# Performance work log

Hardware: AMD Instinct MI355X
Metric: run time of the kernel (lower is better)

Reference implementation:

```python
import jax, jax.numpy as jnp
import numpy as np
import math

EPS = 1e-5

def _ln(x, g, b):
    m = jnp.mean(x, axis=-1, keepdims=True)
    v = jnp.var(x, axis=-1, keepdims=True)
    return (x - m) * jax.lax.rsqrt(v + EPS) * g + b

def _rn_layer(x, W, g, b, A, Bb, Rw):
    # x: (B,S,in) -> (B,S,out). W: (out,in), A: (out,basis), Bb: (basis,out)
    S = x.shape[1]
    basis_dim = Bb.shape[0]
    n = _ln(x @ W.T, g, b)                      # (B,S,out)
    j = jnp.arange(S) % basis_dim               # (S,)
    Bv = Bb[j]                                  # (S,out)
    scal = jnp.einsum('bsd,sd->bs', n, Bv)      # (B,S)
    Av = A[:, j].T                              # (S,out)
    nf = scal[..., None] * Av                   # (B,S,out)
    res = x if Rw is None else x @ Rw.T
    return nf + res

def _ts_layer(x, M, g, b, P, Rw):
    # x: (B,S,in) -> (B,S,out). M: (out,in), P: (out,out,G)
    S = x.shape[1]
    D, _, G = P.shape
    t = _ln(x @ M.T, g, b)                      # (B,S,out)
    k = jnp.arange(S, dtype=jnp.float32)
    periods = (jnp.arange(D, dtype=jnp.float32)[:, None, None] * (D * G)
               + jnp.arange(D, dtype=jnp.float32)[None, :, None] * G
               + jnp.arange(G, dtype=jnp.float32)[None, None, :] + 2.0)  # (D,D,G)
    phi = jnp.cos(2.0 * math.pi * k[:, None, None, None] / periods)       # (S,D,D,G)
    # Nk[b,s,i] = sum_{j,g} P[i,j,g] * t[b,s,j] * phi[s,i,j,g]
    Wp = jnp.einsum('ijg,sijg->sij', P, phi)    # (S,D,D)
    Nk = jnp.einsum('sij,bsj->bsi', Wp, t)      # (B,S,D)
    return Nk + x @ Rw.T

def setup_inputs() -> dict:
    key = jax.random.key(0)
    ks = jax.random.split(key, 16)
    B, S = 2, 2048
    d0, d1, d2 = 512, 64, 512        # input_dim, ts out, final out
    bas1, G, bas3 = 64, 8, 64
    u = lambda k, sh, a: jax.random.uniform(k, sh, jnp.float32, -a, a)
    inp = {
        'x':  jax.random.normal(ks[0], (B, S, d0), jnp.float32),
        # Layer 1: RN 512->512 (in==out -> no residual proj)
        'W1': u(ks[1], (d0, d0), 0.1),
        'g1': jnp.ones((d0,), jnp.float32),
        'b1': jnp.zeros((d0,), jnp.float32),
        'A1': u(ks[2], (d0, bas1), 0.1),
        'B1': u(ks[3], (bas1, d0), 0.1),
        # Layer 2: TS 512->64
        'M2': u(ks[4], (d1, d0), 0.5),
        'g2': jnp.ones((d1,), jnp.float32),
        'b2': jnp.zeros((d1,), jnp.float32),
        'P2': u(ks[5], (d1, d1, G), 0.1),
        'R2': u(ks[6], (d1, d0), 0.1),
        # Layer 3: RN 64->512
        'W3': u(ks[7], (d2, d1), 0.1),
        'g3': jnp.ones((d2,), jnp.float32),
        'b3': jnp.zeros((d2,), jnp.float32),
        'A3': u(ks[8], (d2, bas3), 0.1),
        'B3': u(ks[9], (bas3, d2), 0.1),
        'R3': u(ks[10], (d2, d1), 0.1),
    }
    return inp

def reference(x, W1, g1, b1, A1, B1, M2, g2, b2, P2, R2, W3, g3, b3, A3, B3, R3):
    h = _rn_layer(x, W1, g1, b1, A1, B1, None)   # (B,S,512), identity residual
    h = _ts_layer(h, M2, g2, b2, P2, R2)         # (B,S,64)
    h = _rn_layer(h, W3, g3, b3, A3, B3, R3)     # (B,S,512)
    return h
```

## Files before the change

### kernel.cpp

```cpp
#include <hip/hip_runtime.h>
#include <math.h>

#define SEQ  2048
#define ROWS 4096
#define D0   512
#define D1   64

typedef short bf8 __attribute__((ext_vector_type(8)));
typedef float f4  __attribute__((ext_vector_type(4)));

__device__ __forceinline__ unsigned short f2bf(float f) {
    unsigned u = __float_as_uint(f);
    return (unsigned short)((u + 0x7fffu + ((u >> 16) & 1u)) >> 16);
}
__device__ __forceinline__ float bf2f(unsigned short u) {
    return __uint_as_float((unsigned)u << 16);
}
__device__ __forceinline__ void hilo(float f, unsigned short& h, unsigned short& l) {
    h = f2bf(f);
    float fh = bf2f(h);
    l = f2bf(f - fh);
}
__device__ __forceinline__ void cv4h(unsigned short* dh, int idx, float4 v) {
    ushort4 hv;
    hv.x = f2bf(v.x); hv.y = f2bf(v.y); hv.z = f2bf(v.z); hv.w = f2bf(v.w);
    *(ushort4*)(dh + idx) = hv;
}

__device__ __forceinline__ void async16(const void* g, void* l) {
    __builtin_amdgcn_global_load_lds(
        (const __attribute__((address_space(1))) unsigned int*)g,
        (__attribute__((address_space(3))) unsigned int*)l, 16, 0, 0);
}

__global__ __launch_bounds__(256) void convk(
        const float* __restrict__ x,  const float* __restrict__ W1,
        const float* __restrict__ M2, const float* __restrict__ R2,
        const float* __restrict__ W3, const float* __restrict__ R3,
        const float* __restrict__ A1, const float* __restrict__ A3,
        unsigned short* __restrict__ xh,
        unsigned short* __restrict__ W1h,
        unsigned short* __restrict__ C2h,
        unsigned short* __restrict__ C3h,
        float* __restrict__ A1T, float* __restrict__ A3T) {
    int c = blockIdx.x, tid = threadIdx.x;
    if (c < 1216) {
        const float* src; unsigned short* dh; int off;
        if      (c < 1024) { src = x;  dh = xh;          off = c; }
        else if (c < 1152) { src = W1; dh = W1h;         off = c - 1024; }
        else if (c < 1168) { src = M2; dh = C2h;         off = c - 1152; }
        else if (c < 1184) { src = R2; dh = C2h + 32768; off = c - 1168; }
        else if (c < 1200) { src = W3; dh = C3h;         off = c - 1184; }
        else               { src = R3; dh = C3h + 32768; off = c - 1200; }
        int base = off * 2048 + tid * 4;
        cv4h(dh, base,        *(const float4*)(src + base));
        cv4h(dh, base + 1024, *(const float4*)(src + base + 1024));
    } else {
        int gid = (c - 1216) * 256 + tid;
        int i = gid >> 6, j = gid & 63;
        A1T[j * 512 + i] = A1[gid];
        A3T[j * 512 + i] = A3[gid];
    }
}

template<bool ALO, int OM>
__global__ __launch_bounds__(256, 4) void gemm128t(
        const unsigned short* __restrict__ Ah, const unsigned short* __restrict__ Al,
        const unsigned short* __restrict__ Wh,
        float* __restrict__ Cf, unsigned short* __restrict__ Cb,
        int M, int N, int K, int Ks) {
    __shared__ __align__(16) unsigned short aH[8192];
    __shared__ __align__(16) unsigned short aL[ALO ? 8192 : 16];
    __shared__ __align__(16) unsigned short wH[4096];
    const int tid = threadIdx.x;
    const int wv  = tid >> 6;
    const int ln  = tid & 63;
    const int lm  = ln & 15;
    const int lq  = ln >> 4;
    const int bm  = blockIdx.y * 128;
    const int bn  = blockIdx.x * 64;
    const int k0  = blockIdx.z * Ks;

    f4 acc[2][4] = {};

    for (int kt = 0; kt < Ks; kt += 64) {
        const int kg = k0 + kt;
        __syncthreads();
#pragma unroll
        for (int i = 0; i < 4; ++i) {
            int slot = i * 256 + wv * 64 + ln;
            int row  = slot >> 3;
            int ch   = (slot & 7) ^ (row & 7);
            size_t go = (size_t)(bm + row) * K + kg + ch * 8;
            async16(Ah + go, aH + slot * 8);
            if constexpr (ALO) async16(Al + go, aL + slot * 8);
        }
#pragma unroll
        for (int i = 0; i < 2; ++i) {
            int slot = i * 256 + wv * 64 + ln;
            int row  = slot >> 3;
            int ch   = (slot & 7) ^ (row & 7);
            size_t go = (size_t)(bn + row) * K + kg + ch * 8;
            async16(Wh + go, wH + slot * 8);
        }
        __syncthreads();

#pragma unroll
        for (int kk = 0; kk < 2; ++kk) {
            const int ck = kk * 4 + lq;
            bf8 a_h[2], a_l[2], b_h[4];
#pragma unroll
            for (int t = 0; t < 2; ++t) {
                int r = wv * 32 + t * 16 + lm;
                a_h[t] = *(const bf8*)(aH + r * 64 + ((ck ^ (r & 7)) * 8));
                if constexpr (ALO)
                    a_l[t] = *(const bf8*)(aL + r * 64 + ((ck ^ (r & 7)) * 8));
            }
#pragma unroll
            for (int u = 0; u < 4; ++u) {
                int rb = u * 16 + lm;
                b_h[u] = *(const bf8*)(wH + rb * 64 + ((ck ^ (rb & 7)) * 8));
            }
#pragma unroll
            for (int t = 0; t < 2; ++t)
#pragma unroll
                for (int u = 0; u < 4; ++u) {
                    acc[t][u] = __builtin_amdgcn_mfma_f32_16x16x32_bf16(a_h[t], b_h[u], acc[t][u], 0, 0, 0);
                    if constexpr (ALO)
                        acc[t][u] = __builtin_amdgcn_mfma_f32_16x16x32_bf16(a_l[t], b_h[u], acc[t][u], 0, 0, 0);
                }
        }
    }

#pragma unroll
    for (int t = 0; t < 2; ++t)
#pragma unroll
        for (int u = 0; u < 4; ++u) {
            int row = bm + wv * 32 + t * 16 + lq * 4;
            int col = bn + u * 16 + lm;
#pragma unroll
            for (int r = 0; r < 4; ++r) {
                float v = acc[t][u][r];
                if constexpr (OM == 0) {
                    Cf[(size_t)blockIdx.z * M * N + (size_t)(row + r) * N + col] = v;
                } else if constexpr (OM == 1) {
                    Cb[(size_t)blockIdx.z * M * N + (size_t)(row + r) * N + col] = f2bf(v);
                } else {
                    if (col < 512) Cb[(size_t)(row + r) * 512 + col] = f2bf(v);
                    else           Cf[(size_t)(row + r) * 512 + col - 512] = v;
                }
            }
        }
}

__global__ __launch_bounds__(256) void lnrn(
        const unsigned short* __restrict__ Yb0,
        const unsigned short* __restrict__ Yb1,
        const float* __restrict__ RES,
        const float* __restrict__ g, const float* __restrict__ be,
        const float* __restrict__ Bb, const float* __restrict__ AaT,
        float* __restrict__ outf,
        unsigned short* __restrict__ outh, unsigned short* __restrict__ outl) {
    const int row = blockIdx.x * 4 + (threadIdx.x >> 6);
    const int l = threadIdx.x & 63;
    const int c = l * 8;
    ushort4 ua = *(const ushort4*)(Yb0 + (size_t)row * D0 + c);
    ushort4 ub = *(const ushort4*)(Yb0 + (size_t)row * D0 + c + 4);
    float4 y0, y1;
    y0.x = bf2f(ua.x); y0.y = bf2f(ua.y); y0.z = bf2f(ua.z); y0.w = bf2f(ua.w);
    y1.x = bf2f(ub.x); y1.y = bf2f(ub.y); y1.z = bf2f(ub.z); y1.w = bf2f(ub.w);
    if (Yb1) {
        ushort4 va = *(const ushort4*)(Yb1 + (size_t)row * D0 + c);
        ushort4 vb = *(const ushort4*)(Yb1 + (size_t)row * D0 + c + 4);
        y0.x += bf2f(va.x); y0.y += bf2f(va.y); y0.z += bf2f(va.z); y0.w += bf2f(va.w);
        y1.x += bf2f(vb.x); y1.y += bf2f(vb.y); y1.z += bf2f(vb.z); y1.w += bf2f(vb.w);
    }
    float sum = y0.x + y0.y + y0.z + y0.w + y1.x + y1.y + y1.z + y1.w;
    float ssq = y0.x*y0.x + y0.y*y0.y + y0.z*y0.z + y0.w*y0.w
              + y1.x*y1.x + y1.y*y1.y + y1.z*y1.z + y1.w*y1.w;
#pragma unroll
    for (int m = 1; m < 64; m <<= 1) {
        sum += __shfl_xor(sum, m, 64);
        ssq += __shfl_xor(ssq, m, 64);
    }
    float mean = sum * (1.0f / 512.0f);
    float var  = ssq * (1.0f / 512.0f) - mean * mean;
    float rstd = rsqrtf(var + 1e-5f);
    float4 g0 = *(const float4*)(g + c),  g1v = *(const float4*)(g + c + 4);
    float4 e0 = *(const float4*)(be + c), e1  = *(const float4*)(be + c + 4);
    float4 n0, n1;
    n0.x = (y0.x - mean) * rstd * g0.x  + e0.x;
    n0.y = (y0.y - mean) * rstd * g0.y  + e0.y;
    n0.z = (y0.z - mean) * rstd * g0.z  + e0.z;
    n0.w = (y0.w - mean) * rstd * g0.w  + e0.w;
    n1.x = (y1.x - mean) * rstd * g1v.x + e1.x;
    n1.y = (y1.y - mean) * rstd * g1v.y + e1.y;
    n1.z = (y1.z - mean) * rstd * g1v.z + e1.z;
    n1.w = (y1.w - mean) * rstd * g1v.w + e1.w;
    const int jm = row & 63;
    const float* bb = Bb + jm * D0 + c;
    float4 b0 = *(const float4*)bb, b1v = *(const float4*)(bb + 4);
    float p = n0.x*b0.x + n0.y*b0.y + n0.z*b0.z + n0.w*b0.w
            + n1.x*b1v.x + n1.y*b1v.y + n1.z*b1v.z + n1.w*b1v.w;
#pragma unroll
    for (int m = 1; m < 64; m <<= 1) p += __shfl_xor(p, m, 64);
    const float* av = AaT + jm * D0 + c;
    float4 a0 = *(const float4*)av, a1 = *(const float4*)(av + 4);
    const float* rs = RES + (size_t)row * D0 + c;
    float4 r0 = *(const float4*)rs, r1 = *(const float4*)(rs + 4);
    float4 v0, v1;
    v0.x = p*a0.x + r0.x; v0.y = p*a0.y + r0.y; v0.z = p*a0.z + r0.z; v0.w = p*a0.w + r0.w;
    v1.x = p*a1.x + r1.x; v1.y = p*a1.y + r1.y; v1.z = p*a1.z + r1.z; v1.w = p*a1.w + r1.w;
    if (outf) {
        *(float4*)(outf + (size_t)row * D0 + c)     = v0;
        *(float4*)(outf + (size_t)row * D0 + c + 4) = v1;
    } else {
        ushort4 h0, l0, h1, l1;
        hilo(v0.x, h0.x, l0.x); hilo(v0.y, h0.y, l0.y);
        hilo(v0.z, h0.z, l0.z); hilo(v0.w, h0.w, l0.w);
        hilo(v1.x, h1.x, l1.x); hilo(v1.y, h1.y, l1.y);
        hilo(v1.z, h1.z, l1.z); hilo(v1.w, h1.w, l1.w);
        *(ushort4*)(outh + (size_t)row * D0 + c)     = h0;
        *(ushort4*)(outl + (size_t)row * D0 + c)     = l0;
        *(ushort4*)(outh + (size_t)row * D0 + c + 4) = h1;
        *(ushort4*)(outl + (size_t)row * D0 + c + 4) = l1;
    }
}

#define C2S 524288
__global__ __launch_bounds__(256) void lnt(
        const float* __restrict__ C2, const float* __restrict__ g2,
        const float* __restrict__ b2,
        float* __restrict__ t, float* __restrict__ rsum) {
    const int r = blockIdx.x * 4 + (threadIdx.x >> 6);
    const int j = threadIdx.x & 63;
    size_t base = (size_t)r * 128 + j;
    float v = 0.f, rv = 0.f;
#pragma unroll
    for (int z = 0; z < 4; ++z) {
        v  += C2[(size_t)z * C2S + base];
        rv += C2[(size_t)z * C2S + base + 64];
    }
    float sum = v, ssq = v * v;
#pragma unroll
    for (int m = 1; m < 64; m <<= 1) {
        sum += __shfl_xor(sum, m, 64);
        ssq += __shfl_xor(ssq, m, 64);
    }
    float mean = sum * (1.0f / 64.0f);
    float var  = ssq * (1.0f / 64.0f) - mean * mean;
    float rstd = rsqrtf(var + 1e-5f);
    t[r * 64 + j]    = (v - mean) * rstd * g2[j] + b2[j];
    rsum[r * 64 + j] = rv;
}

__global__ __launch_bounds__(256) void tsk2(
        const float* __restrict__ t, const float* __restrict__ rsum,
        const float* __restrict__ P,
        unsigned short* __restrict__ Hh, unsigned short* __restrict__ Hl) {
    const int bid = blockIdx.x;
    const int i   = bid >> 3;
    const int sg  = bid & 7;
    const int w   = threadIdx.x >> 6;
    const int ln  = threadIdx.x & 63;
    const int s0  = sg * 256 + w * 64;
    const int idx = i * 64 + ln;
    const float* pp = P + idx * 8;
    const float sf0 = (float)s0;

    float k2c[8], ca[8], cb[8];
#pragma unroll
    for (int g = 0; g < 8; ++g) {
        float pf   = (float)(idx * 8 + g + 2);
        float invp = __builtin_amdgcn_rcpf(pf);
        k2c[g] = 2.0f * __builtin_amdgcn_cosf(invp);
        float q0 = floorf(sf0 * invp);
        float r0 = fmaf(-q0, pf, sf0);
        float f0 = r0 * invp; f0 -= floorf(f0);
        float c0 = __builtin_amdgcn_cosf(f0);
        float sf1 = sf0 + 1.0f;
        float q1 = floorf(sf1 * invp);
        float r1 = fmaf(-q1, pf, sf1);
        float f1 = r1 * invp; f1 -= floorf(f1);
        float c1 = __builtin_amdgcn_cosf(f1);
        float Pv = pp[g];
        ca[g] = Pv * c0;
        cb[g] = Pv * c1;
    }

    const int tb = s0 * 64 + ln;
    float t0c = t[tb], t1c = t[131072 + tb];
    float res0 = 0.f, res1 = 0.f;

    for (int st = 0; st < 64; st += 2) {
        float t0n  = t[tb + (st + 1) * 64];
        float t1n  = t[131072 + tb + (st + 1) * 64];
        float ws = ((ca[0] + ca[1]) + (ca[2] + ca[3]))
                 + ((ca[4] + ca[5]) + (ca[6] + ca[7]));
#pragma unroll
        for (int g = 0; g < 8; ++g) ca[g] = fmaf(k2c[g], cb[g], -ca[g]);
        float v0 = ws * t0c, v1 = ws * t1c;
#pragma unroll
        for (int m = 1; m < 64; m <<= 1) {
            v0 += __shfl_xor(v0, m, 64);
            v1 += __shfl_xor(v1, m, 64);
        }
        res0 = (ln == st) ? v0 : res0;
        res1 = (ln == st) ? v1 : res1;
        float t0n2 = t[tb + (st + 2) * 64];
        float t1n2 = t[131072 + tb + (st + 2) * 64];
        float ws2 = ((cb[0] + cb[1]) + (cb[2] + cb[3]))
                  + ((cb[4] + cb[5]) + (cb[6] + cb[7]));
#pragma unroll
        for (int g = 0; g < 8; ++g) cb[g] = fmaf(k2c[g], ca[g], -cb[g]);
        float v0b = ws2 * t0n, v1b = ws2 * t1n;
#pragma unroll
        for (int m = 1; m < 64; m <<= 1) {
            v0b += __shfl_xor(v0b, m, 64);
            v1b += __shfl_xor(v1b, m, 64);
        }
        res0 = (ln == st + 1) ? v0b : res0;
        res1 = (ln == st + 1) ? v1b : res1;
        t0c = t0n2; t1c = t1n2;
    }

    const int s = s0 + ln;
    {
        float v = res0 + rsum[(size_t)s * 64 + i];
        unsigned short h, l; hilo(v, h, l);
        Hh[(size_t)s * 64 + i] = h; Hl[(size_t)s * 64 + i] = l;
        float v1e = res1 + rsum[(size_t)(SEQ + s) * 64 + i];
        hilo(v1e, h, l);
        Hh[(size_t)(SEQ + s) * 64 + i] = h; Hl[(size_t)(SEQ + s) * 64 + i] = l;
    }
}

extern "C" void kernel_launch(void* const* d_in, const int* in_sizes, int n_in,
                              void* d_out, int out_size, void* d_ws, size_t ws_size,
                              hipStream_t stream) {
    const float* x  = (const float*)d_in[0];
    const float* W1 = (const float*)d_in[1];
    const float* g1 = (const float*)d_in[2];
    const float* b1 = (const float*)d_in[3];
    const float* A1 = (const float*)d_in[4];
    const float* B1 = (const float*)d_in[5];
    const float* M2 = (const float*)d_in[6];
    const float* g2 = (const float*)d_in[7];
    const float* b2 = (const float*)d_in[8];
    const float* P2 = (const float*)d_in[9];
    const float* R2 = (const float*)d_in[10];
    const float* W3 = (const float*)d_in[11];
    const float* g3 = (const float*)d_in[12];
    const float* b3 = (const float*)d_in[13];
    const float* A3 = (const float*)d_in[14];
    const float* B3 = (const float*)d_in[15];
    const float* R3 = (const float*)d_in[16];

    float* ws = (float*)d_ws;
    float* C2   = ws;
    float* C3r  = ws + 2097152;
    float* t    = ws + 4194304;
    float* rsum = ws + 4456448;
    float* A1T  = ws + 4718592;
    float* A3T  = ws + 4751360;
    unsigned short* us = (unsigned short*)(ws + 4784128);
    unsigned short* xh   = us;
    unsigned short* h1h  = us + 2097152;
    unsigned short* h1l  = us + 4194304;
    unsigned short* W1h  = us + 6291456;
    unsigned short* Wc2h = us + 6553600;
    unsigned short* Wc3h = us + 6619136;
    unsigned short* h2h  = us + 6684672;
    unsigned short* h2l  = us + 6946816;
    unsigned short* C1b  = us + 7208960;
    unsigned short* C3n  = us + 11403264;

    dim3 blk(256);

    convk<<<1344, blk, 0, stream>>>(x, W1, M2, R2, W3, R3, A1, A3,
                                    xh, W1h, Wc2h, Wc3h, A1T, A3T);

    gemm128t<false, 1><<<dim3(8, 32, 2), blk, 0, stream>>>(
        xh, xh, W1h, nullptr, C1b, ROWS, 512, 512, 256);
    lnrn<<<1024, blk, 0, stream>>>(C1b, C1b + (size_t)ROWS * 512, x,
                                   g1, b1, B1, A1T, nullptr, h1h, h1l);

    gemm128t<true, 0><<<dim3(2, 32, 4), blk, 0, stream>>>(
        h1h, h1l, Wc2h, C2, nullptr, ROWS, 128, 512, 128);
    lnt<<<1024, blk, 0, stream>>>(C2, g2, b2, t, rsum);
    tsk2<<<512, blk, 0, stream>>>(t, rsum, P2, h2h, h2l);

    gemm128t<true, 2><<<dim3(16, 32, 1), blk, 0, stream>>>(
        h2h, h2l, Wc3h, C3r, C3n, ROWS, 1024, 64, 64);
    lnrn<<<1024, blk, 0, stream>>>(C3n, nullptr, C3r, g3, b3, B3, A3T,
                                   (float*)d_out, nullptr, nullptr);
}
```

Before: 152.1 us.

## Fold layer-1 output algebraically into layer-2 GEMM via precomputed A1·M2 products

Layer 1's output h1 = x + scal·A1[:,j] is linear in x, so its product with the layer-2 weights M2/R2 becomes x·M2ᵀ plus scal times a precomputed 64x64 table G = A1ᵀ·M2 (built inside the conversion kernel). One GEMM now computes both x·W1ᵀ and x·[M2;R2]ᵀ together, and a new fused kernel does LN1, the scalar projection, and LN2. This removes the h1 hi/lo materialization, a separate GEMM launch and the lnt kernel. In exchange, x is split into hi/lo bf16, with the lo pass applied only to the M2/R2 column blocks. A runtime branch replaces the compile-time low-part switch in the GEMM.

```diff
diff --git a/kernel.cpp b/kernel.cpp
--- a/kernel.cpp
+++ b/kernel.cpp
@@ -5,6 +5,7 @@
 #define ROWS 4096
 #define D0   512
 #define D1   64
+#define C2S  524288
 
 typedef short bf8 __attribute__((ext_vector_type(8)));
 typedef float f4  __attribute__((ext_vector_type(4)));
@@ -38,16 +39,28 @@
         const float* __restrict__ M2, const float* __restrict__ R2,
         const float* __restrict__ W3, const float* __restrict__ R3,
         const float* __restrict__ A1, const float* __restrict__ A3,
-        unsigned short* __restrict__ xh,
+        unsigned short* __restrict__ xh, unsigned short* __restrict__ xl,
         unsigned short* __restrict__ W1h,
         unsigned short* __restrict__ C2h,
         unsigned short* __restrict__ C3h,
-        float* __restrict__ A1T, float* __restrict__ A3T) {
+        float* __restrict__ A3T,
+        float* __restrict__ G2y, float* __restrict__ G2r) {
+    __shared__ float sh[4][64];
     int c = blockIdx.x, tid = threadIdx.x;
-    if (c < 1216) {
+    if (c < 1024) {
+        int base = c * 2048 + tid * 4;
+        float4 v0 = *(const float4*)(x + base);
+        float4 v1 = *(const float4*)(x + base + 1024);
+        ushort4 h, l;
+        hilo(v0.x, h.x, l.x); hilo(v0.y, h.y, l.y);
+        hilo(v0.z, h.z, l.z); hilo(v0.w, h.w, l.w);
+        *(ushort4*)(xh + base) = h; *(ushort4*)(xl + base) = l;
+        hilo(v1.x, h.x, l.x); hilo(v1.y, h.y, l.y);
+        hilo(v1.z, h.z, l.z); hilo(v1.w, h.w, l.w);
+        *(ushort4*)(xh + base + 1024) = h; *(ushort4*)(xl + base + 1024) = l;
+    } else if (c < 1216) {
         const float* src; unsigned short* dh; int off;
-        if      (c < 1024) { src = x;  dh = xh;          off = c; }
-        else if (c < 1152) { src = W1; dh = W1h;         off = c - 1024; }
+        if      (c < 1152) { src = W1; dh = W1h;         off = c - 1024; }
         else if (c < 1168) { src = M2; dh = C2h;         off = c - 1152; }
         else if (c < 1184) { src = R2; dh = C2h + 32768; off = c - 1168; }
         else if (c < 1200) { src = W3; dh = C3h;         off = c - 1184; }
@@ -55,23 +68,36 @@
         int base = off * 2048 + tid * 4;
         cv4h(dh, base,        *(const float4*)(src + base));
         cv4h(dh, base + 1024, *(const float4*)(src + base + 1024));
-    } else {
+    } else if (c < 1344) {
         int gid = (c - 1216) * 256 + tid;
         int i = gid >> 6, j = gid & 63;
-        A1T[j * 512 + i] = A1[gid];
         A3T[j * 512 + i] = A3[gid];
-    }
-}
-
-template<bool ALO, int OM>
+    } else {
+        int jrow = (c - 1344) & 63;
+        const float* wv = (c < 1408) ? (M2 + jrow * 512) : (R2 + jrow * 512);
+        float* G = (c < 1408) ? G2y : G2r;
+        int jm = tid & 63, q = tid >> 6;
+        const float* ap = A1 + (q * 128) * 64 + jm;
+        const float* wp = wv + q * 128;
+        float acc = 0.f;
+        for (int cc = 0; cc < 128; ++cc)
+            acc = fmaf(ap[cc * 64], wp[cc], acc);
+        sh[q][jm] = acc;
+        __syncthreads();
+        if (tid < 64)
+            G[tid * 64 + jrow] = (sh[0][tid] + sh[1][tid]) + (sh[2][tid] + sh[3][tid]);
+    }
+}
+
+template<int AMODE, int OM>
 __global__ __launch_bounds__(256, 4) void gemm128t(
         const unsigned short* __restrict__ Ah, const unsigned short* __restrict__ Al,
         const unsigned short* __restrict__ Wh,
         float* __restrict__ Cf, unsigned short* __restrict__ Cb,
-        int M, int N, int K, int Ks) {
+        int N, int K, int Ks) {
     __shared__ __align__(16) unsigned short aH[8192];
-    __shared__ __align__(16) unsigned short aL[ALO ? 8192 : 16];
-    __shared__ __align__(16) unsigned short wH[4096];
+    __shared__ __align__(16) unsigned short aL[AMODE ? 8192 : 16];
+    __shared__ __align__(16) unsigned short wHs[4096];
     const int tid = threadIdx.x;
     const int wv  = tid >> 6;
     const int ln  = tid & 63;
@@ -80,6 +106,7 @@
     const int bm  = blockIdx.y * 128;
     const int bn  = blockIdx.x * 64;
     const int k0  = blockIdx.z * Ks;
+    const bool alo = (AMODE == 1) || (AMODE == 2 && bn >= 512);
 
     f4 acc[2][4] = {};
 
@@ -93,7 +120,7 @@
             int ch   = (slot & 7) ^ (row & 7);
             size_t go = (size_t)(bm + row) * K + kg + ch * 8;
             async16(Ah + go, aH + slot * 8);
-            if constexpr (ALO) async16(Al + go, aL + slot * 8);
+            if (alo) async16(Al + go, aL + slot * 8);
         }
 #pragma unroll
         for (int i = 0; i < 2; ++i) {
@@ -101,7 +128,7 @@
             int row  = slot >> 3;
             int ch   = (slot & 7) ^ (row & 7);
             size_t go = (size_t)(bn + row) * K + kg + ch * 8;
-            async16(Wh + go, wH + slot * 8);
+            async16(Wh + go, wHs + slot * 8);
         }
         __syncthreads();
 
@@ -113,20 +140,20 @@
             for (int t = 0; t < 2; ++t) {
                 int r = wv * 32 + t * 16 + lm;
                 a_h[t] = *(const bf8*)(aH + r * 64 + ((ck ^ (r & 7)) * 8));
-                if constexpr (ALO)
+                if (alo)
                     a_l[t] = *(const bf8*)(aL + r * 64 + ((ck ^ (r & 7)) * 8));
             }
 #pragma unroll
             for (int u = 0; u < 4; ++u) {
                 int rb = u * 16 + lm;
-                b_h[u] = *(const bf8*)(wH + rb * 64 + ((ck ^ (rb & 7)) * 8));
+                b_h[u] = *(const bf8*)(wHs + rb * 64 + ((ck ^ (rb & 7)) * 8));
             }
 #pragma unroll
             for (int t = 0; t < 2; ++t)
 #pragma unroll
                 for (int u = 0; u < 4; ++u) {
                     acc[t][u] = __builtin_amdgcn_mfma_f32_16x16x32_bf16(a_h[t], b_h[u], acc[t][u], 0, 0, 0);
-                    if constexpr (ALO)
+                    if (alo)
                         acc[t][u] = __builtin_amdgcn_mfma_f32_16x16x32_bf16(a_l[t], b_h[u], acc[t][u], 0, 0, 0);
                 }
         }
@@ -141,26 +168,95 @@
 #pragma unroll
             for (int r = 0; r < 4; ++r) {
                 float v = acc[t][u][r];
-                if constexpr (OM == 0) {
-                    Cf[(size_t)blockIdx.z * M * N + (size_t)(row + r) * N + col] = v;
-                } else if constexpr (OM == 1) {
-                    Cb[(size_t)blockIdx.z * M * N + (size_t)(row + r) * N + col] = f2bf(v);
-                } else {
+                if constexpr (OM == 2) {
                     if (col < 512) Cb[(size_t)(row + r) * 512 + col] = f2bf(v);
                     else           Cf[(size_t)(row + r) * 512 + col - 512] = v;
+                } else {
+                    if (col < 512)
+                        Cb[(size_t)blockIdx.z * ROWS * 512 + (size_t)(row + r) * 512 + col] = f2bf(v);
+                    else
+                        Cf[(size_t)blockIdx.z * ROWS * 128 + (size_t)(row + r) * 128 + (col - 512)] = v;
                 }
             }
         }
 }
 
+__global__ __launch_bounds__(256) void ptk(
+        const unsigned short* __restrict__ C1b,
+        const float* __restrict__ C2,
+        const float* __restrict__ B1,
+        const float* __restrict__ g1, const float* __restrict__ b1,
+        const float* __restrict__ g2, const float* __restrict__ b2,
+        const float* __restrict__ G2y, const float* __restrict__ G2r,
+        float* __restrict__ t, float* __restrict__ rsum) {
+    const int row = blockIdx.x * 4 + (threadIdx.x >> 6);
+    const int l = threadIdx.x & 63;
+    const int c = l * 8;
+    const int jm = row & 63;
+    const size_t rb0 = (size_t)row * 512 + c;
+    ushort4 ua = *(const ushort4*)(C1b + rb0);
+    ushort4 ub = *(const ushort4*)(C1b + rb0 + 4);
+    ushort4 va = *(const ushort4*)(C1b + (size_t)ROWS * 512 + rb0);
+    ushort4 vb = *(const ushort4*)(C1b + (size_t)ROWS * 512 + rb0 + 4);
+    float y[8];
+    y[0] = bf2f(ua.x) + bf2f(va.x); y[1] = bf2f(ua.y) + bf2f(va.y);
+    y[2] = bf2f(ua.z) + bf2f(va.z); y[3] = bf2f(ua.w) + bf2f(va.w);
+    y[4] = bf2f(ub.x) + bf2f(vb.x); y[5] = bf2f(ub.y) + bf2f(vb.y);
+    y[6] = bf2f(ub.z) + bf2f(vb.z); y[7] = bf2f(ub.w) + bf2f(vb.w);
+    float4 B0  = *(const float4*)(B1 + jm * 512 + c);
+    float4 B1q = *(const float4*)(B1 + jm * 512 + c + 4);
+    float4 gg0 = *(const float4*)(g1 + c), gg1 = *(const float4*)(g1 + c + 4);
+    float4 bb0 = *(const float4*)(b1 + c), bb1 = *(const float4*)(b1 + c + 4);
+    float Bv[8] = {B0.x, B0.y, B0.z, B0.w, B1q.x, B1q.y, B1q.z, B1q.w};
+    float gv[8] = {gg0.x, gg0.y, gg0.z, gg0.w, gg1.x, gg1.y, gg1.z, gg1.w};
+    float bv[8] = {bb0.x, bb0.y, bb0.z, bb0.w, bb1.x, bb1.y, bb1.z, bb1.w};
+    float sum = 0.f, ssq = 0.f, S1 = 0.f, SU = 0.f, SBB = 0.f;
+#pragma unroll
+    for (int i = 0; i < 8; ++i) {
+        float u = gv[i] * Bv[i];
+        sum += y[i];
+        ssq = fmaf(y[i], y[i], ssq);
+        S1  = fmaf(y[i], u, S1);
+        SU  += u;
+        SBB = fmaf(bv[i], Bv[i], SBB);
+    }
+#pragma unroll
+    for (int m = 1; m < 64; m <<= 1) {
+        sum += __shfl_xor(sum, m, 64);
+        ssq += __shfl_xor(ssq, m, 64);
+        S1  += __shfl_xor(S1, m, 64);
+        SU  += __shfl_xor(SU, m, 64);
+        SBB += __shfl_xor(SBB, m, 64);
+    }
+    float mean = sum * (1.0f / 512.0f);
+    float var  = ssq * (1.0f / 512.0f) - mean * mean;
+    float rstd = rsqrtf(var + 1e-5f);
+    float p = rstd * (S1 - mean * SU) + SBB;
+
+    const size_t rb = (size_t)row * 128;
+    float z  = C2[rb + l]      + C2[C2S + rb + l];
+    float zr = C2[rb + 64 + l] + C2[C2S + rb + 64 + l];
+    float v  = z  + p * G2y[jm * 64 + l];
+    float rv = zr + p * G2r[jm * 64 + l];
+    float s2 = v, q2 = v * v;
+#pragma unroll
+    for (int m = 1; m < 64; m <<= 1) {
+        s2 += __shfl_xor(s2, m, 64);
+        q2 += __shfl_xor(q2, m, 64);
+    }
+    float mean2 = s2 * (1.0f / 64.0f);
+    float var2  = q2 * (1.0f / 64.0f) - mean2 * mean2;
+    float rstd2 = rsqrtf(var2 + 1e-5f);
+    t[row * 64 + l]    = (v - mean2) * rstd2 * g2[l] + b2[l];
+    rsum[row * 64 + l] = rv;
+}
+
 __global__ __launch_bounds__(256) void lnrn(
         const unsigned short* __restrict__ Yb0,
-        const unsigned short* __restrict__ Yb1,
         const float* __restrict__ RES,
         const float* __restrict__ g, const float* __restrict__ be,
         const float* __restrict__ Bb, const float* __restrict__ AaT,
-        float* __restrict__ outf,
-        unsigned short* __restrict__ outh, unsigned short* __restrict__ outl) {
+        float* __restrict__ outf) {
     const int row = blockIdx.x * 4 + (threadIdx.x >> 6);
     const int l = threadIdx.x & 63;
     const int c = l * 8;
@@ -169,12 +265,6 @@
     float4 y0, y1;
     y0.x = bf2f(ua.x); y0.y = bf2f(ua.y); y0.z = bf2f(ua.z); y0.w = bf2f(ua.w);
     y1.x = bf2f(ub.x); y1.y = bf2f(ub.y); y1.z = bf2f(ub.z); y1.w = bf2f(ub.w);
-    if (Yb1) {
-        ushort4 va = *(const ushort4*)(Yb1 + (size_t)row * D0 + c);
-        ushort4 vb = *(const ushort4*)(Yb1 + (size_t)row * D0 + c + 4);
-        y0.x += bf2f(va.x); y0.y += bf2f(va.y); y0.z += bf2f(va.z); y0.w += bf2f(va.w);
-        y1.x += bf2f(vb.x); y1.y += bf2f(vb.y); y1.z += bf2f(vb.z); y1.w += bf2f(vb.w);
-    }
     float sum = y0.x + y0.y + y0.z + y0.w + y1.x + y1.y + y1.z + y1.w;
     float ssq = y0.x*y0.x + y0.y*y0.y + y0.z*y0.z + y0.w*y0.w
               + y1.x*y1.x + y1.y*y1.y + y1.z*y1.z + y1.w*y1.w;
@@ -211,47 +301,8 @@
     float4 v0, v1;
     v0.x = p*a0.x + r0.x; v0.y = p*a0.y + r0.y; v0.z = p*a0.z + r0.z; v0.w = p*a0.w + r0.w;
     v1.x = p*a1.x + r1.x; v1.y = p*a1.y + r1.y; v1.z = p*a1.z + r1.z; v1.w = p*a1.w + r1.w;
-    if (outf) {
-        *(float4*)(outf + (size_t)row * D0 + c)     = v0;
-        *(float4*)(outf + (size_t)row * D0 + c + 4) = v1;
-    } else {
-        ushort4 h0, l0, h1, l1;
-        hilo(v0.x, h0.x, l0.x); hilo(v0.y, h0.y, l0.y);
-        hilo(v0.z, h0.z, l0.z); hilo(v0.w, h0.w, l0.w);
-        hilo(v1.x, h1.x, l1.x); hilo(v1.y, h1.y, l1.y);
-        hilo(v1.z, h1.z, l1.z); hilo(v1.w, h1.w, l1.w);
-        *(ushort4*)(outh + (size_t)row * D0 + c)     = h0;
-        *(ushort4*)(outl + (size_t)row * D0 + c)     = l0;
-        *(ushort4*)(outh + (size_t)row * D0 + c + 4) = h1;
-        *(ushort4*)(outl + (size_t)row * D0 + c + 4) = l1;
-    }
-}
-
-#define C2S 524288
-__global__ __launch_bounds__(256) void lnt(
-        const float* __restrict__ C2, const float* __restrict__ g2,
-        const float* __restrict__ b2,
-        float* __restrict__ t, float* __restrict__ rsum) {
-    const int r = blockIdx.x * 4 + (threadIdx.x >> 6);
-    const int j = threadIdx.x & 63;
-    size_t base = (size_t)r * 128 + j;
-    float v = 0.f, rv = 0.f;
-#pragma unroll
-    for (int z = 0; z < 4; ++z) {
-        v  += C2[(size_t)z * C2S + base];
-        rv += C2[(size_t)z * C2S + base + 64];
-    }
-    float sum = v, ssq = v * v;
-#pragma unroll
-    for (int m = 1; m < 64; m <<= 1) {
-        sum += __shfl_xor(sum, m, 64);
-        ssq += __shfl_xor(ssq, m, 64);
-    }
-    float mean = sum * (1.0f / 64.0f);
-    float var  = ssq * (1.0f / 64.0f) - mean * mean;
-    float rstd = rsqrtf(var + 1e-5f);
-    t[r * 64 + j]    = (v - mean) * rstd * g2[j] + b2[j];
-    rsum[r * 64 + j] = rv;
+    *(float4*)(outf + (size_t)row * D0 + c)     = v0;
+    *(float4*)(outf + (size_t)row * D0 + c + 4) = v1;
 }
 
 __global__ __launch_bounds__(256) void tsk2(
@@ -338,6 +389,7 @@
 extern "C" void kernel_launch(void* const* d_in, const int* in_sizes, int n_in,
                               void* d_out, int out_size, void* d_ws, size_t ws_size,
                               hipStream_t stream) {
+    (void)in_sizes; (void)n_in; (void)out_size; (void)ws_size;
     const float* x  = (const float*)d_in[0];
     const float* W1 = (const float*)d_in[1];
     const float* g1 = (const float*)d_in[2];
@@ -361,12 +413,12 @@
     float* C3r  = ws + 2097152;
     float* t    = ws + 4194304;
     float* rsum = ws + 4456448;
-    float* A1T  = ws + 4718592;
+    float* G2y  = ws + 4718592;
+    float* G2r  = ws + 4722688;
     float* A3T  = ws + 4751360;
     unsigned short* us = (unsigned short*)(ws + 4784128);
     unsigned short* xh   = us;
-    unsigned short* h1h  = us + 2097152;
-    unsigned short* h1l  = us + 4194304;
+    unsigned short* xl   = us + 2097152;
     unsigned short* W1h  = us + 6291456;
     unsigned short* Wc2h = us + 6553600;
     unsigned short* Wc3h = us + 6619136;
@@ -377,21 +429,18 @@
 
     dim3 blk(256);
 
-    convk<<<1344, blk, 0, stream>>>(x, W1, M2, R2, W3, R3, A1, A3,
-                                    xh, W1h, Wc2h, Wc3h, A1T, A3T);
-
-    gemm128t<false, 1><<<dim3(8, 32, 2), blk, 0, stream>>>(
-        xh, xh, W1h, nullptr, C1b, ROWS, 512, 512, 256);
-    lnrn<<<1024, blk, 0, stream>>>(C1b, C1b + (size_t)ROWS * 512, x,
-                                   g1, b1, B1, A1T, nullptr, h1h, h1l);
-
-    gemm128t<true, 0><<<dim3(2, 32, 4), blk, 0, stream>>>(
-        h1h, h1l, Wc2h, C2, nullptr, ROWS, 128, 512, 128);
-    lnt<<<1024, blk, 0, stream>>>(C2, g2, b2, t, rsum);
+    convk<<<1472, blk, 0, stream>>>(x, W1, M2, R2, W3, R3, A1, A3,
+                                    xh, xl, W1h, Wc2h, Wc3h, A3T, G2y, G2r);
+
+    gemm128t<2, 3><<<dim3(10, 32, 2), blk, 0, stream>>>(
+        xh, xl, W1h, C2, C1b, 640, 512, 256);
+
+    ptk<<<1024, blk, 0, stream>>>(C1b, C2, B1, g1, b1, g2, b2, G2y, G2r, t, rsum);
+
     tsk2<<<512, blk, 0, stream>>>(t, rsum, P2, h2h, h2l);
 
-    gemm128t<true, 2><<<dim3(16, 32, 1), blk, 0, stream>>>(
-        h2h, h2l, Wc3h, C3r, C3n, ROWS, 1024, 64, 64);
-    lnrn<<<1024, blk, 0, stream>>>(C3n, nullptr, C3r, g3, b3, B3, A3T,
-                                   (float*)d_out, nullptr, nullptr);
-}
+    gemm128t<1, 2><<<dim3(16, 32, 1), blk, 0, stream>>>(
+        h2h, h2l, Wc3h, C3r, C3n, 1024, 64, 64);
+
+    lnrn<<<1024, blk, 0, stream>>>(C3n, C3r, g3, b3, B3, A3T, (float*)d_out);
+}
```

Result: faster. 146.7 us (-3.6%).
